# Kernel tuning notes

Measured on AMD Instinct MI355X. Metric: run time of the kernel, lower is better.

Reference implementation:

```python
import math
import jax, jax.numpy as jnp
import numpy as np

B, L, D, H = 4, 2048, 1024, 16
KD = D // H

def setup_inputs() -> dict:
    key = jax.random.key(0)
    k1, k2, k3 = jax.random.split(key, 3)
    x = jax.random.normal(k1, (B, L, D), dtype=jnp.float32)
    pad_mask = jnp.zeros((B, L), dtype=bool)  # True = padded (masked) key position
    w_qkv = jax.random.normal(k2, (D, 3 * D), dtype=jnp.float32) / math.sqrt(D)
    w_out = jax.random.normal(k3, (D, D), dtype=jnp.float32) / math.sqrt(D)
    return {"x": x, "pad_mask": pad_mask, "w_qkv": w_qkv, "w_out": w_out}

def reference(x, pad_mask, w_qkv, w_out):
    Bx, Lx, Dx = x.shape
    qkv = jnp.einsum('bld,de->ble', x, w_qkv)          # [B,L,3D]
    q, k, v = jnp.split(qkv, 3, axis=-1)
    def heads(t):
        return t.reshape(Bx, Lx, H, KD).transpose(0, 2, 1, 3)  # [B,H,L,kd]
    qh, kh, vh = heads(q), heads(k), heads(v)
    scores = jnp.einsum('bhqd,bhkd->bhqk', qh, kh) / math.sqrt(KD)
    causal = jnp.triu(jnp.ones((Lx, Lx), dtype=bool), k=1)[None, None]   # [1,1,L,L]
    mask = causal | pad_mask[:, None, None, :]                            # [B,1,L,L]
    scores = jnp.where(mask, -jnp.inf, scores)
    probs = jax.nn.softmax(scores, axis=-1)
    att = jnp.einsum('bhqk,bhkd->bhqd', probs, vh)
    concat = att.transpose(0, 2, 1, 3).reshape(Bx, Lx, Dx)
    return jnp.einsum('bld,de->ble', concat, w_out)
```

## Files before the change

### kernel.cpp

```cpp
#include <hip/hip_runtime.h>
#include <hip/hip_bf16.h>
#include <math.h>


typedef __bf16 bf16x8 __attribute__((ext_vector_type(8)));
typedef float f32x4 __attribute__((ext_vector_type(4)));

__device__ __forceinline__ f32x4 mfma16(bf16x8 a, bf16x8 b, f32x4 c) {
    return __builtin_amdgcn_mfma_f32_16x16x32_bf16(a, b, c, 0, 0, 0);
}

__device__ __forceinline__ void async16(const void* g, void* l) {
    __builtin_amdgcn_global_load_lds(
        (const __attribute__((address_space(1))) unsigned int*)g,
        (__attribute__((address_space(3))) unsigned int*)l, 16, 0, 0);
}

__global__ void cvt_f32_bf16_v4(const float* __restrict__ in,
                                __hip_bfloat16* __restrict__ out, int n4) {
    int i = blockIdx.x * blockDim.x + threadIdx.x;
    if (i >= n4) return;
    float4 v = ((const float4*)in)[i];
    __hip_bfloat16 t[4];
    t[0] = __float2bfloat16(v.x);
    t[1] = __float2bfloat16(v.y);
    t[2] = __float2bfloat16(v.z);
    t[3] = __float2bfloat16(v.w);
    ((uint2*)out)[i] = *(uint2*)t;
}

__global__ void transpose_cvt(const float* __restrict__ W,
                              __hip_bfloat16* __restrict__ Wt, int K, int N) {
    __shared__ float tile[32][33];
    int tid = threadIdx.x;
    int tx = tid & 31, ty = tid >> 5;
    int n0 = blockIdx.x * 32, k0 = blockIdx.y * 32;
#pragma unroll
    for (int i = 0; i < 4; ++i)
        tile[ty + 8 * i][tx] = W[(size_t)(k0 + ty + 8 * i) * N + n0 + tx];
    __syncthreads();
#pragma unroll
    for (int i = 0; i < 4; ++i)
        Wt[(size_t)(n0 + ty + 8 * i) * K + k0 + tx] =
            __float2bfloat16(tile[tx][ty + 8 * i]);
}

template <int MODE>
__global__ __launch_bounds__(256) void gemm_bf16(
    const __hip_bfloat16* __restrict__ A, const __hip_bfloat16* __restrict__ Bt,
    float* __restrict__ Cf, __hip_bfloat16* __restrict__ Qo,
    __hip_bfloat16* __restrict__ Ko, __hip_bfloat16* __restrict__ Vto, int M,
    int N, int K) {
    __shared__ __hip_bfloat16 As[128 * 32];
    __shared__ __hip_bfloat16 Bs[128 * 32];
    int tid = threadIdx.x;
    int wave = tid >> 6, lane = tid & 63;
    int quad = lane >> 4, l16 = lane & 15;
    int m0 = blockIdx.x * 128, n0 = blockIdx.y * 128;
    int wm = (wave >> 1) * 64, wn = (wave & 1) * 64;
    int srow = lane >> 2, scol = (lane & 3) * 8;
    f32x4 acc[4][4] = {};
    for (int k0 = 0; k0 < K; k0 += 32) {
        __syncthreads();
#pragma unroll
        for (int j = 0; j < 2; ++j) {
            int r0 = (j * 4 + wave) * 16;
            async16(&A[(size_t)(m0 + r0 + srow) * K + k0 + scol], &As[r0 * 32]);
            async16(&Bt[(size_t)(n0 + r0 + srow) * K + k0 + scol], &Bs[r0 * 32]);
        }
        __syncthreads();
        bf16x8 af[4], bfr[4];
#pragma unroll
        for (int i = 0; i < 4; ++i) {
            af[i]  = *(const bf16x8*)&As[(wm + i * 16 + l16) * 32 + quad * 8];
            bfr[i] = *(const bf16x8*)&Bs[(wn + i * 16 + l16) * 32 + quad * 8];
        }
#pragma unroll
        for (int mi = 0; mi < 4; ++mi)
#pragma unroll
            for (int ni = 0; ni < 4; ++ni)
                acc[mi][ni] = mfma16(af[mi], bfr[ni], acc[mi][ni]);
    }
#pragma unroll
    for (int mi = 0; mi < 4; ++mi) {
#pragma unroll
        for (int ni = 0; ni < 4; ++ni) {
            int row0 = m0 + wm + mi * 16 + quad * 4;
            int col = n0 + wn + ni * 16 + l16;
            if (MODE == 0) {
#pragma unroll
                for (int r = 0; r < 4; ++r)
                    Cf[(size_t)(row0 + r) * N + col] = acc[mi][ni][r];
            } else {
                int which = col >> 10, hd = col & 1023;
                int h = hd >> 6, d = hd & 63;
                if (which == 0) {
#pragma unroll
                    for (int r = 0; r < 4; ++r) {
                        int row = row0 + r;
                        int b = row >> 11, l = row & 2047;
                        Qo[(((size_t)b * 16 + h) * 2048 + l) * 64 + d] =
                            __float2bfloat16(acc[mi][ni][r] * 0.18033688011f);
                    }
                } else if (which == 1) {
#pragma unroll
                    for (int r = 0; r < 4; ++r) {
                        int row = row0 + r;
                        int b = row >> 11, l = row & 2047;
                        Ko[(((size_t)b * 16 + h) * 2048 + l) * 64 + d] =
                            __float2bfloat16(acc[mi][ni][r]);
                    }
                } else {
                    int b = row0 >> 11, l = row0 & 2047;
                    __hip_bfloat16 t4[4];
#pragma unroll
                    for (int r = 0; r < 4; ++r)
                        t4[r] = __float2bfloat16(acc[mi][ni][r]);
                    *(uint2*)&Vto[(((size_t)b * 16 + h) * 64 + d) * 2048 + l] =
                        *(uint2*)t4;
                }
            }
        }
    }
}

__global__ __launch_bounds__(256, 2) void attn_kernel(
    const __hip_bfloat16* __restrict__ Q, const __hip_bfloat16* __restrict__ Kk,
    const __hip_bfloat16* __restrict__ Vt,
    const unsigned char* __restrict__ pm, __hip_bfloat16* __restrict__ Ao) {
    constexpr int LD = 72;
    __shared__ __hip_bfloat16 Ks[64 * LD];
    __shared__ __hip_bfloat16 Vs[64 * LD];
    __shared__ __hip_bfloat16 Ps[4 * 32 * LD];
    __shared__ unsigned char pmS[2048];
    int tid = threadIdx.x;
    int wave = tid >> 6, lane = tid & 63;
    int quad = lane >> 4, l16 = lane & 15;
    int bx = blockIdx.x;
    int bh = blockIdx.y;
    int b = bh >> 4, h = bh & 15;
    const __hip_bfloat16* Qbh = Q + (size_t)bh * 2048 * 64;
    const __hip_bfloat16* Kbh = Kk + (size_t)bh * 2048 * 64;
    const __hip_bfloat16* Vbh = Vt + (size_t)bh * 64 * 2048;
    *(uint2*)&pmS[tid * 8] = *(const uint2*)&pm[b * 2048 + tid * 8];
    int srow = tid >> 2, scol = (tid & 3) * 16;

#pragma unroll
    for (int ph = 0; ph < 2; ++ph) {
        int qt = ph ? bx : 15 - bx;
        bf16x8 qf[2][2];
#pragma unroll
        for (int mi = 0; mi < 2; ++mi) {
            int qrow = qt * 128 + (wave + 4 * mi) * 16 + l16;
#pragma unroll
            for (int c = 0; c < 2; ++c)
                qf[mi][c] =
                    *(const bf16x8*)&Qbh[(size_t)qrow * 64 + c * 32 + quad * 8];
        }
        f32x4 ov[2][4] = {};
        float lacc[2][4] = {};
        int ktmax = 2 * qt + 1;
        uint4 kr0 = *(const uint4*)&Kbh[(size_t)srow * 64 + scol];
        uint4 kr1 = *(const uint4*)&Kbh[(size_t)srow * 64 + scol + 8];
        uint4 vr0 = *(const uint4*)&Vbh[(size_t)srow * 2048 + scol];
        uint4 vr1 = *(const uint4*)&Vbh[(size_t)srow * 2048 + scol + 8];
        for (int kt = 0; kt <= ktmax; ++kt) {
            __syncthreads();
            *(uint4*)&Ks[srow * LD + scol] = kr0;
            *(uint4*)&Ks[srow * LD + scol + 8] = kr1;
            *(uint4*)&Vs[srow * LD + scol] = vr0;
            *(uint4*)&Vs[srow * LD + scol + 8] = vr1;
            if (kt < ktmax) {
                kr0 = *(const uint4*)&Kbh[((size_t)(kt + 1) * 64 + srow) * 64 + scol];
                kr1 = *(const uint4*)&Kbh[((size_t)(kt + 1) * 64 + srow) * 64 + scol + 8];
                vr0 = *(const uint4*)&Vbh[(size_t)srow * 2048 + (kt + 1) * 64 + scol];
                vr1 = *(const uint4*)&Vbh[(size_t)srow * 2048 + (kt + 1) * 64 + scol + 8];
            }
            __syncthreads();
            float sc[2][4][4];
#pragma unroll
            for (int kn = 0; kn < 4; ++kn) {
                bf16x8 b0 = *(const bf16x8*)&Ks[(kn * 16 + l16) * LD + quad * 8];
                bf16x8 b1 =
                    *(const bf16x8*)&Ks[(kn * 16 + l16) * LD + 32 + quad * 8];
                float bias = pmS[kt * 64 + kn * 16 + l16] ? -INFINITY : -8.0f;
#pragma unroll
                for (int mi = 0; mi < 2; ++mi) {
                    f32x4 s = {};
                    s = mfma16(qf[mi][0], b0, s);
                    s = mfma16(qf[mi][1], b1, s);
#pragma unroll
                    for (int r = 0; r < 4; ++r) sc[mi][kn][r] = s[r] + bias;
                }
            }
            if (kt >= 2 * qt) {
#pragma unroll
                for (int mi = 0; mi < 2; ++mi) {
                    int qbase = qt * 128 + (wave + 4 * mi) * 16 + quad * 4;
#pragma unroll
                    for (int kn = 0; kn < 4; ++kn) {
                        int key = kt * 64 + kn * 16 + l16;
#pragma unroll
                        for (int r = 0; r < 4; ++r)
                            if (key > qbase + r) sc[mi][kn][r] = -INFINITY;
                    }
                }
            }
            __hip_bfloat16* Pw = Ps + wave * 32 * LD;
#pragma unroll
            for (int mi = 0; mi < 2; ++mi)
#pragma unroll
                for (int kn = 0; kn < 4; ++kn)
#pragma unroll
                    for (int r = 0; r < 4; ++r) {
                        float p = __builtin_amdgcn_exp2f(sc[mi][kn][r]);
                        __hip_bfloat16 pb = __float2bfloat16(p);
                        Pw[(mi * 16 + quad * 4 + r) * LD + kn * 16 + l16] = pb;
                        lacc[mi][r] += __bfloat162float(pb);
                    }
            bf16x8 pf[2][2];
#pragma unroll
            for (int mi = 0; mi < 2; ++mi)
#pragma unroll
                for (int c = 0; c < 2; ++c)
                    pf[mi][c] = *(const bf16x8*)&Pw[(mi * 16 + l16) * LD +
                                                    c * 32 + quad * 8];
#pragma unroll
            for (int ni = 0; ni < 4; ++ni) {
                bf16x8 v0 = *(const bf16x8*)&Vs[(ni * 16 + l16) * LD + quad * 8];
                bf16x8 v1 =
                    *(const bf16x8*)&Vs[(ni * 16 + l16) * LD + 32 + quad * 8];
#pragma unroll
                for (int mi = 0; mi < 2; ++mi) {
                    ov[mi][ni] = mfma16(pf[mi][0], v0, ov[mi][ni]);
                    ov[mi][ni] = mfma16(pf[mi][1], v1, ov[mi][ni]);
                }
            }
        }
#pragma unroll
        for (int mi = 0; mi < 2; ++mi)
#pragma unroll
            for (int r = 0; r < 4; ++r) {
                float rs = lacc[mi][r];
#pragma unroll
                for (int off = 1; off < 16; off <<= 1)
                    rs += __shfl_xor(rs, off);
                float inv = 1.0f / rs;
                int qrow = qt * 128 + (wave + 4 * mi) * 16 + quad * 4 + r;
#pragma unroll
                for (int ni = 0; ni < 4; ++ni)
                    Ao[(size_t)(b * 2048 + qrow) * 1024 + h * 64 + ni * 16 +
                       l16] = __float2bfloat16(ov[mi][ni][r] * inv);
            }
    }
}

extern "C" void kernel_launch(void* const* d_in, const int* in_sizes, int n_in,
                              void* d_out, int out_size, void* d_ws,
                              size_t ws_size, hipStream_t stream) {
    (void)in_sizes; (void)n_in; (void)out_size; (void)ws_size;
    const float* x = (const float*)d_in[0];
    const unsigned char* pm = (const unsigned char*)d_in[1];
    const float* wqkv = (const float*)d_in[2];
    const float* wout = (const float*)d_in[3];
    float* out = (float*)d_out;

    char* p = (char*)d_ws;
    auto alloc = [&](size_t bytes) {
        char* q = p;
        p += (bytes + 255) & ~(size_t)255;
        return q;
    };
    __hip_bfloat16* xb    = (__hip_bfloat16*)alloc((size_t)8192 * 1024 * 2);
    __hip_bfloat16* wqkvT = (__hip_bfloat16*)alloc((size_t)3072 * 1024 * 2);
    __hip_bfloat16* woutT = (__hip_bfloat16*)alloc((size_t)1024 * 1024 * 2);
    __hip_bfloat16* qws   = (__hip_bfloat16*)alloc((size_t)8192 * 1024 * 2);
    __hip_bfloat16* kws   = (__hip_bfloat16*)alloc((size_t)8192 * 1024 * 2);
    __hip_bfloat16* vtws  = (__hip_bfloat16*)alloc((size_t)8192 * 1024 * 2);
    __hip_bfloat16* attb  = (__hip_bfloat16*)alloc((size_t)8192 * 1024 * 2);

    cvt_f32_bf16_v4<<<8192, 256, 0, stream>>>(x, xb, 8192 * 1024 / 4);
    transpose_cvt<<<dim3(3072 / 32, 1024 / 32), 256, 0, stream>>>(wqkv, wqkvT,
                                                                  1024, 3072);
    transpose_cvt<<<dim3(1024 / 32, 1024 / 32), 256, 0, stream>>>(wout, woutT,
                                                                  1024, 1024);
    gemm_bf16<1><<<dim3(64, 24), 256, 0, stream>>>(xb, wqkvT, nullptr, qws, kws,
                                                   vtws, 8192, 3072, 1024);
    attn_kernel<<<dim3(8, 64), 256, 0, stream>>>(qws, kws, vtws, pm, attb);
    gemm_bf16<0><<<dim3(64, 8), 256, 0, stream>>>(attb, woutT, out, nullptr,
                                                  nullptr, nullptr, 8192, 1024,
                                                  1024);
}
```

Baseline: 260.4 us.

## Swizzle LDS tiles, deepen GEMM K-step, and halve attention query tile

The GEMM K-step grows from 32 to 64, and its LDS tiles use an XOR swizzle so async global-to-LDS loads and MFMA fragment reads avoid bank conflicts without padding. The attention kernel drops from 128-query to 64-query tiles, one 16-row slice per wave. The grid doubles and the occupancy hint is removed. Attention K/V staging moves from register prefetch to direct async loads into swizzled LDS. This trades less K/V reuse per block and the loss of register double-buffering for more parallelism, lower register pressure and conflict-free LDS access.

```diff
diff --git a/kernel.cpp b/kernel.cpp
--- a/kernel.cpp
+++ b/kernel.cpp
@@ -51,35 +51,43 @@
     float* __restrict__ Cf, __hip_bfloat16* __restrict__ Qo,
     __hip_bfloat16* __restrict__ Ko, __hip_bfloat16* __restrict__ Vto, int M,
     int N, int K) {
-    __shared__ __hip_bfloat16 As[128 * 32];
-    __shared__ __hip_bfloat16 Bs[128 * 32];
+    __shared__ __hip_bfloat16 As[128 * 64];
+    __shared__ __hip_bfloat16 Bs[128 * 64];
     int tid = threadIdx.x;
     int wave = tid >> 6, lane = tid & 63;
     int quad = lane >> 4, l16 = lane & 15;
     int m0 = blockIdx.x * 128, n0 = blockIdx.y * 128;
     int wm = (wave >> 1) * 64, wn = (wave & 1) * 64;
-    int srow = lane >> 2, scol = (lane & 3) * 8;
+    int srow = lane >> 3;
+    int g8 = ((lane & 7) ^ srow) * 8;
+    int swz = (l16 & 7);
     f32x4 acc[4][4] = {};
-    for (int k0 = 0; k0 < K; k0 += 32) {
+    for (int k0 = 0; k0 < K; k0 += 64) {
         __syncthreads();
 #pragma unroll
-        for (int j = 0; j < 2; ++j) {
-            int r0 = (j * 4 + wave) * 16;
-            async16(&A[(size_t)(m0 + r0 + srow) * K + k0 + scol], &As[r0 * 32]);
-            async16(&Bt[(size_t)(n0 + r0 + srow) * K + k0 + scol], &Bs[r0 * 32]);
+        for (int j = 0; j < 4; ++j) {
+            int r0 = (j * 4 + wave) * 8;
+            async16(&A[(size_t)(m0 + r0 + srow) * K + k0 + g8], &As[r0 * 64]);
+            async16(&Bt[(size_t)(n0 + r0 + srow) * K + k0 + g8], &Bs[r0 * 64]);
         }
         __syncthreads();
-        bf16x8 af[4], bfr[4];
-#pragma unroll
-        for (int i = 0; i < 4; ++i) {
-            af[i]  = *(const bf16x8*)&As[(wm + i * 16 + l16) * 32 + quad * 8];
-            bfr[i] = *(const bf16x8*)&Bs[(wn + i * 16 + l16) * 32 + quad * 8];
-        }
-#pragma unroll
-        for (int mi = 0; mi < 4; ++mi)
-#pragma unroll
-            for (int ni = 0; ni < 4; ++ni)
-                acc[mi][ni] = mfma16(af[mi], bfr[ni], acc[mi][ni]);
+        bf16x8 af[2][4], bfr[2][4];
+#pragma unroll
+        for (int c = 0; c < 2; ++c) {
+            int pg = ((c * 4 + quad) ^ swz) * 8;
+#pragma unroll
+            for (int i = 0; i < 4; ++i) {
+                af[c][i]  = *(const bf16x8*)&As[(wm + i * 16 + l16) * 64 + pg];
+                bfr[c][i] = *(const bf16x8*)&Bs[(wn + i * 16 + l16) * 64 + pg];
+            }
+        }
+#pragma unroll
+        for (int c = 0; c < 2; ++c)
+#pragma unroll
+            for (int mi = 0; mi < 4; ++mi)
+#pragma unroll
+                for (int ni = 0; ni < 4; ++ni)
+                    acc[mi][ni] = mfma16(af[c][mi], bfr[c][ni], acc[mi][ni]);
     }
 #pragma unroll
     for (int mi = 0; mi < 4; ++mi) {
@@ -124,18 +132,21 @@
     }
 }
 
-__global__ __launch_bounds__(256, 2) void attn_kernel(
+__global__ __launch_bounds__(256) void attn_kernel(
     const __hip_bfloat16* __restrict__ Q, const __hip_bfloat16* __restrict__ Kk,
     const __hip_bfloat16* __restrict__ Vt,
     const unsigned char* __restrict__ pm, __hip_bfloat16* __restrict__ Ao) {
-    constexpr int LD = 72;
-    __shared__ __hip_bfloat16 Ks[64 * LD];
-    __shared__ __hip_bfloat16 Vs[64 * LD];
-    __shared__ __hip_bfloat16 Ps[4 * 32 * LD];
+    __shared__ __hip_bfloat16 Ks[64 * 64];
+    __shared__ __hip_bfloat16 Vs[64 * 64];
+    constexpr int LDP = 72;
+    __shared__ __hip_bfloat16 Ps[4 * 16 * LDP];
     __shared__ unsigned char pmS[2048];
     int tid = threadIdx.x;
     int wave = tid >> 6, lane = tid & 63;
     int quad = lane >> 4, l16 = lane & 15;
+    int srow = lane >> 3;
+    int g8 = ((lane & 7) ^ srow) * 8;
+    int swz = (l16 & 7);
     int bx = blockIdx.x;
     int bh = blockIdx.y;
     int b = bh >> 4, h = bh & 15;
@@ -143,115 +154,86 @@
     const __hip_bfloat16* Kbh = Kk + (size_t)bh * 2048 * 64;
     const __hip_bfloat16* Vbh = Vt + (size_t)bh * 64 * 2048;
     *(uint2*)&pmS[tid * 8] = *(const uint2*)&pm[b * 2048 + tid * 8];
-    int srow = tid >> 2, scol = (tid & 3) * 16;
+    __hip_bfloat16* Pw = Ps + wave * 16 * LDP;
 
 #pragma unroll
     for (int ph = 0; ph < 2; ++ph) {
-        int qt = ph ? bx : 15 - bx;
-        bf16x8 qf[2][2];
-#pragma unroll
-        for (int mi = 0; mi < 2; ++mi) {
-            int qrow = qt * 128 + (wave + 4 * mi) * 16 + l16;
-#pragma unroll
-            for (int c = 0; c < 2; ++c)
-                qf[mi][c] =
-                    *(const bf16x8*)&Qbh[(size_t)qrow * 64 + c * 32 + quad * 8];
-        }
-        f32x4 ov[2][4] = {};
-        float lacc[2][4] = {};
-        int ktmax = 2 * qt + 1;
-        uint4 kr0 = *(const uint4*)&Kbh[(size_t)srow * 64 + scol];
-        uint4 kr1 = *(const uint4*)&Kbh[(size_t)srow * 64 + scol + 8];
-        uint4 vr0 = *(const uint4*)&Vbh[(size_t)srow * 2048 + scol];
-        uint4 vr1 = *(const uint4*)&Vbh[(size_t)srow * 2048 + scol + 8];
-        for (int kt = 0; kt <= ktmax; ++kt) {
+        int qt = ph ? bx : 31 - bx;
+        int q0 = qt * 64;
+        bf16x8 qf[2];
+        {
+            int qrow = q0 + wave * 16 + l16;
+            qf[0] = *(const bf16x8*)&Qbh[(size_t)qrow * 64 + quad * 8];
+            qf[1] = *(const bf16x8*)&Qbh[(size_t)qrow * 64 + 32 + quad * 8];
+        }
+        f32x4 ov[4] = {};
+        float lacc[4] = {};
+        for (int kt = 0; kt <= qt; ++kt) {
             __syncthreads();
-            *(uint4*)&Ks[srow * LD + scol] = kr0;
-            *(uint4*)&Ks[srow * LD + scol + 8] = kr1;
-            *(uint4*)&Vs[srow * LD + scol] = vr0;
-            *(uint4*)&Vs[srow * LD + scol + 8] = vr1;
-            if (kt < ktmax) {
-                kr0 = *(const uint4*)&Kbh[((size_t)(kt + 1) * 64 + srow) * 64 + scol];
-                kr1 = *(const uint4*)&Kbh[((size_t)(kt + 1) * 64 + srow) * 64 + scol + 8];
-                vr0 = *(const uint4*)&Vbh[(size_t)srow * 2048 + (kt + 1) * 64 + scol];
-                vr1 = *(const uint4*)&Vbh[(size_t)srow * 2048 + (kt + 1) * 64 + scol + 8];
+#pragma unroll
+            for (int j = 0; j < 2; ++j) {
+                int r0 = (j * 4 + wave) * 8;
+                async16(&Kbh[((size_t)kt * 64 + r0 + srow) * 64 + g8],
+                        &Ks[r0 * 64]);
+                async16(&Vbh[(size_t)(r0 + srow) * 2048 + kt * 64 + g8],
+                        &Vs[r0 * 64]);
             }
             __syncthreads();
-            float sc[2][4][4];
+            float sc[4][4];
 #pragma unroll
             for (int kn = 0; kn < 4; ++kn) {
-                bf16x8 b0 = *(const bf16x8*)&Ks[(kn * 16 + l16) * LD + quad * 8];
-                bf16x8 b1 =
-                    *(const bf16x8*)&Ks[(kn * 16 + l16) * LD + 32 + quad * 8];
+                int row = (kn * 16 + l16) * 64;
+                bf16x8 b0 = *(const bf16x8*)&Ks[row + ((quad ^ swz) * 8)];
+                bf16x8 b1 = *(const bf16x8*)&Ks[row + (((4 + quad) ^ swz) * 8)];
                 float bias = pmS[kt * 64 + kn * 16 + l16] ? -INFINITY : -8.0f;
-#pragma unroll
-                for (int mi = 0; mi < 2; ++mi) {
-                    f32x4 s = {};
-                    s = mfma16(qf[mi][0], b0, s);
-                    s = mfma16(qf[mi][1], b1, s);
-#pragma unroll
-                    for (int r = 0; r < 4; ++r) sc[mi][kn][r] = s[r] + bias;
+                f32x4 s = {};
+                s = mfma16(qf[0], b0, s);
+                s = mfma16(qf[1], b1, s);
+#pragma unroll
+                for (int r = 0; r < 4; ++r) sc[kn][r] = s[r] + bias;
+            }
+            if (kt == qt) {
+                int qbase = wave * 16 + quad * 4;
+#pragma unroll
+                for (int kn = 0; kn < 4; ++kn) {
+                    int key = kn * 16 + l16;
+#pragma unroll
+                    for (int r = 0; r < 4; ++r)
+                        if (key > qbase + r) sc[kn][r] = -INFINITY;
                 }
             }
-            if (kt >= 2 * qt) {
-#pragma unroll
-                for (int mi = 0; mi < 2; ++mi) {
-                    int qbase = qt * 128 + (wave + 4 * mi) * 16 + quad * 4;
-#pragma unroll
-                    for (int kn = 0; kn < 4; ++kn) {
-                        int key = kt * 64 + kn * 16 + l16;
-#pragma unroll
-                        for (int r = 0; r < 4; ++r)
-                            if (key > qbase + r) sc[mi][kn][r] = -INFINITY;
-                    }
+#pragma unroll
+            for (int kn = 0; kn < 4; ++kn)
+#pragma unroll
+                for (int r = 0; r < 4; ++r) {
+                    float p = __builtin_amdgcn_exp2f(sc[kn][r]);
+                    __hip_bfloat16 pb = __float2bfloat16(p);
+                    Pw[(quad * 4 + r) * LDP + kn * 16 + l16] = pb;
+                    lacc[r] += __bfloat162float(pb);
                 }
-            }
-            __hip_bfloat16* Pw = Ps + wave * 32 * LD;
-#pragma unroll
-            for (int mi = 0; mi < 2; ++mi)
-#pragma unroll
-                for (int kn = 0; kn < 4; ++kn)
-#pragma unroll
-                    for (int r = 0; r < 4; ++r) {
-                        float p = __builtin_amdgcn_exp2f(sc[mi][kn][r]);
-                        __hip_bfloat16 pb = __float2bfloat16(p);
-                        Pw[(mi * 16 + quad * 4 + r) * LD + kn * 16 + l16] = pb;
-                        lacc[mi][r] += __bfloat162float(pb);
-                    }
-            bf16x8 pf[2][2];
-#pragma unroll
-            for (int mi = 0; mi < 2; ++mi)
-#pragma unroll
-                for (int c = 0; c < 2; ++c)
-                    pf[mi][c] = *(const bf16x8*)&Pw[(mi * 16 + l16) * LD +
-                                                    c * 32 + quad * 8];
+            bf16x8 pf0 = *(const bf16x8*)&Pw[l16 * LDP + quad * 8];
+            bf16x8 pf1 = *(const bf16x8*)&Pw[l16 * LDP + 32 + quad * 8];
 #pragma unroll
             for (int ni = 0; ni < 4; ++ni) {
-                bf16x8 v0 = *(const bf16x8*)&Vs[(ni * 16 + l16) * LD + quad * 8];
-                bf16x8 v1 =
-                    *(const bf16x8*)&Vs[(ni * 16 + l16) * LD + 32 + quad * 8];
-#pragma unroll
-                for (int mi = 0; mi < 2; ++mi) {
-                    ov[mi][ni] = mfma16(pf[mi][0], v0, ov[mi][ni]);
-                    ov[mi][ni] = mfma16(pf[mi][1], v1, ov[mi][ni]);
-                }
-            }
-        }
-#pragma unroll
-        for (int mi = 0; mi < 2; ++mi)
-#pragma unroll
-            for (int r = 0; r < 4; ++r) {
-                float rs = lacc[mi][r];
-#pragma unroll
-                for (int off = 1; off < 16; off <<= 1)
-                    rs += __shfl_xor(rs, off);
-                float inv = 1.0f / rs;
-                int qrow = qt * 128 + (wave + 4 * mi) * 16 + quad * 4 + r;
-#pragma unroll
-                for (int ni = 0; ni < 4; ++ni)
-                    Ao[(size_t)(b * 2048 + qrow) * 1024 + h * 64 + ni * 16 +
-                       l16] = __float2bfloat16(ov[mi][ni][r] * inv);
-            }
+                int row = (ni * 16 + l16) * 64;
+                bf16x8 v0 = *(const bf16x8*)&Vs[row + ((quad ^ swz) * 8)];
+                bf16x8 v1 = *(const bf16x8*)&Vs[row + (((4 + quad) ^ swz) * 8)];
+                ov[ni] = mfma16(pf0, v0, ov[ni]);
+                ov[ni] = mfma16(pf1, v1, ov[ni]);
+            }
+        }
+#pragma unroll
+        for (int r = 0; r < 4; ++r) {
+            float rs = lacc[r];
+#pragma unroll
+            for (int off = 1; off < 16; off <<= 1) rs += __shfl_xor(rs, off);
+            float inv = 1.0f / rs;
+            int qrow = q0 + wave * 16 + quad * 4 + r;
+#pragma unroll
+            for (int ni = 0; ni < 4; ++ni)
+                Ao[(size_t)(b * 2048 + qrow) * 1024 + h * 64 + ni * 16 + l16] =
+                    __float2bfloat16(ov[ni][r] * inv);
+        }
     }
 }
 
@@ -286,7 +268,7 @@
                                                                   1024, 1024);
     gemm_bf16<1><<<dim3(64, 24), 256, 0, stream>>>(xb, wqkvT, nullptr, qws, kws,
                                                    vtws, 8192, 3072, 1024);
-    attn_kernel<<<dim3(8, 64), 256, 0, stream>>>(qws, kws, vtws, pm, attb);
+    attn_kernel<<<dim3(16, 64), 256, 0, stream>>>(qws, kws, vtws, pm, attb);
     gemm_bf16<0><<<dim3(64, 8), 256, 0, stream>>>(attb, woutT, out, nullptr,
                                                   nullptr, nullptr, 8192, 1024,
                                                   1024);
```

Result: no change. 257.8 us (-1.0%).
